# Kernel optimization log

Measured on AMD Instinct MI355X. Metric: run time of the kernel, lower is better.

Reference implementation:

```python
import jax, jax.numpy as jnp
import numpy as np

N = 10000      # num nodes
DEG = 8        # avg out-degree
E = N * DEG    # num bonds (directed edges)
D_IN = 128; D_HID = 128; D_OUT = 128; H = 16; HD = D_OUT // H
NG = 20; G_STOP = 10.0   # GaussianSmearing: 20 gaussians on [0, 10]
NF = 3                   # AngularEncoding num_funcs -> 1 + 4*NF = 13 feats


def _triplets(row, col, n):
    # numpy replica of BondUpdateLayer.triplets (SparseTensor version):
    # for each edge e=(j=row[e] -> i=col[e]), enumerate edges e'=(k -> j), drop k==i.
    order = np.argsort(col, kind='stable')          # edges sorted by target node
    in_count = np.bincount(col, minlength=n)
    in_start = np.concatenate([np.zeros(1, np.int64), np.cumsum(in_count)])
    num_t = in_count[row]                           # triplets per edge e
    T = int(num_t.sum())
    idx_ji = np.repeat(np.arange(row.size), num_t)
    within = np.arange(T) - np.repeat(np.cumsum(num_t) - num_t, num_t)
    idx_kj = order[in_start[row[idx_ji]] + within]
    idx_k = row[idx_kj]
    idx_i = col[idx_ji]
    idx_j = row[idx_ji]
    mask = idx_i != idx_k
    return idx_i[mask], idx_j[mask], idx_k[mask], idx_kj[mask], idx_ji[mask]


def setup_inputs() -> dict:
    key = jax.random.key(0)
    ks = jax.random.split(key, 8)
    rng = np.random.default_rng(0)
    src = np.repeat(np.arange(N), DEG)
    dst = (src + rng.integers(1, N, size=E)) % N    # random targets, never self-loop
    i_i, i_j, i_k, i_kj, i_ji = _triplets(src, dst, N)
    kv_dim = D_IN + 2 * NG + (1 + 4 * NF)           # 128 + 40 + 13 = 181

    def mlp_params(k, din):
        k1, k2 = jax.random.split(k)
        return {
            'W1': jax.random.normal(k1, (din, D_HID)) * 0.05, 'b1': jnp.zeros(D_HID),
            'g': jnp.ones(D_HID), 'b': jnp.zeros(D_HID),
            'W2': jax.random.normal(k2, (D_HID, D_OUT)) * 0.05, 'b2': jnp.zeros(D_OUT),
        }

    inp = {
        'h': jax.random.normal(ks[3], (N, D_IN)),
        'h_bond': jax.random.normal(ks[4], (E, D_IN)),
        'pos': jax.random.normal(ks[5], (N, 3)) * 3.0,
    }
    for name, k, din in (('hk', ks[0], kv_dim), ('hv', ks[1], kv_dim), ('hq', ks[2], D_IN)):
        for pn, v in mlp_params(k, din).items():
            inp[f'{name}_{pn}'] = v
    inp['bond_row'] = jnp.asarray(src, jnp.int32)
    inp['bond_col'] = jnp.asarray(dst, jnp.int32)
    inp['idx_i'] = jnp.asarray(i_i, jnp.int32)
    inp['idx_j'] = jnp.asarray(i_j, jnp.int32)
    inp['idx_k'] = jnp.asarray(i_k, jnp.int32)
    inp['idx_kj'] = jnp.asarray(i_kj, jnp.int32)
    inp['idx_ji'] = jnp.asarray(i_ji, jnp.int32)
    return inp


def _gauss(d):
    off = jnp.linspace(0.0, G_STOP, NG)
    coeff = -0.5 / (off[1] - off[0]) ** 2
    return jnp.exp(coeff * (d[:, None] - off) ** 2)


def _ang(a):
    freqs = jnp.asarray([1.0, 2.0, 3.0, 1.0, 0.5, 1.0 / 3.0])   # [i+1] + [1/(i+1)]
    x = a[:, None] * freqs
    return jnp.concatenate([a[:, None], jnp.sin(x), jnp.cos(x)], -1)


def _mlp(x, W1, b1, g, b, W2, b2):
    # Linear -> LayerNorm -> ReLU -> Linear
    hdn = x @ W1 + b1
    mu = hdn.mean(-1, keepdims=True)
    var = ((hdn - mu) ** 2).mean(-1, keepdims=True)
    hdn = jax.nn.relu(g * (hdn - mu) * jax.lax.rsqrt(var + 1e-5) + b)
    return hdn @ W2 + b2


def _forward(h, h_bond, pos,
             hk_W1, hk_b1, hk_g, hk_b, hk_W2, hk_b2,
             hv_W1, hv_b1, hv_g, hv_b, hv_W2, hv_b2,
             hq_W1, hq_b1, hq_g, hq_b, hq_W2, hq_b2,
             bond_row, bond_col, idx_i, idx_j, idx_k, idx_kj, idx_ji):
    # per-edge distance features (i=col, j=row in the torch code)
    dist = jnp.linalg.norm(pos[bond_col] - pos[bond_row], axis=-1)   # [E]
    r_feat = _gauss(dist)                                            # [E, 20]
    # per-triplet angle features
    pi = pos[idx_i]
    pji = pos[idx_j] - pi
    pki = pos[idx_k] - pi
    a = (pji * pki).sum(-1)
    bcr = jnp.linalg.norm(jnp.cross(pji, pki), axis=-1)
    a_feat = _ang(jnp.arctan2(bcr, a))                               # [T, 13]
    kv = jnp.concatenate([h_bond[idx_kj], r_feat[idx_kj], r_feat[idx_ji], a_feat], -1)  # [T, 181]
    T = kv.shape[0]
    k = _mlp(kv, hk_W1, hk_b1, hk_g, hk_b, hk_W2, hk_b2).reshape(T, H, HD)
    v = _mlp(kv, hv_W1, hv_b1, hv_g, hv_b, hv_W2, hv_b2).reshape(T, H, HD)
    q = _mlp(h_bond[idx_ji], hq_W1, hq_b1, hq_g, hq_b, hq_W2, hq_b2).reshape(T, H, HD)
    logits = (q * k).sum(-1) / np.sqrt(HD)                           # [T, H]
    # scatter_softmax over idx_ji (segments = edges)
    mx = jax.ops.segment_max(logits, idx_ji, num_segments=E)
    ex = jnp.exp(logits - mx[idx_ji])
    den = jax.ops.segment_sum(ex, idx_ji, num_segments=E)
    alpha = ex / den[idx_ji]                                         # [T, H]
    out = jax.ops.segment_sum(alpha[:, :, None] * v, idx_ji, num_segments=E)  # [E, H, HD]
    return out.reshape(E, D_OUT)


def reference(h, h_bond, pos,
              hk_W1, hk_b1, hk_g, hk_b, hk_W2, hk_b2,
              hv_W1, hv_b1, hv_g, hv_b, hv_W2, hv_b2,
              hq_W1, hq_b1, hq_g, hq_b, hq_W2, hq_b2,
              bond_row, bond_col, idx_i, idx_j, idx_k, idx_kj, idx_ji):
    return _forward(h, h_bond, pos,
                    hk_W1, hk_b1, hk_g, hk_b, hk_W2, hk_b2,
                    hv_W1, hv_b1, hv_g, hv_b, hv_W2, hv_b2,
                    hq_W1, hq_b1, hq_g, hq_b, hq_W2, hq_b2,
                    bond_row, bond_col, idx_i, idx_j, idx_k, idx_kj, idx_ji)
```

## Files before the change

kernel.cpp:

```cpp
#include <hip/hip_runtime.h>
#include <hip/hip_bf16.h>
#include <math.h>

typedef __hip_bfloat16 bf16;
typedef unsigned int u32;

__device__ __forceinline__ float b2f(bf16 x){ return __bfloat162float(x); }
__device__ __forceinline__ bf16  f2b(float x){ return __float2bfloat16(x); }
__device__ __forceinline__ float lo16(u32 u){ return __uint_as_float(u << 16); }
__device__ __forceinline__ float hi16(u32 u){ return __uint_as_float(u & 0xFFFF0000u); }
__device__ __forceinline__ u32 bfbits(float x){
    u32 u = __float_as_uint(x);
    return (u + 0x7FFFu + ((u >> 16) & 1u)) >> 16;
}

#define RSQRT8 0.35355339059327373f
#define G_STEP (10.0f/19.0f)
#define G_COEF (-0.5f/(G_STEP*G_STEP))

__device__ __forceinline__ constexpr int PERM4(int h){
    return ((h&1)<<3) | ((h&2)<<1) | ((h&4)>>1) | ((h&8)>>3);
}

__device__ __forceinline__ float fast_atan2(float y, float x){
    float ax = fabsf(x);
    float mn = fminf(y, ax), mx = fmaxf(y, ax);
    float t = mn / fmaxf(mx, 1e-30f);
    float s = t*t;
    float p = t * (0.99997726f + s*(-0.33262347f + s*(0.19354346f +
              s*(-0.11643287f + s*(0.05265332f + s*(-0.01172120f))))));
    float r = (y > ax) ? (1.5707963267948966f - p) : p;
    r = (x < 0.f) ? (3.14159265358979323f - r) : r;
    return r;
}


__global__ void seg_start_kernel(const int* __restrict__ idx_ji, int T,
                                 int* __restrict__ seg, int E)
{
    int e = blockIdx.x * blockDim.x + threadIdx.x;
    if (e > E) return;
    int lo = 0, hi = T;
    while (lo < hi) { int mid = (lo + hi) >> 1; if (idx_ji[mid] < e) lo = mid + 1; else hi = mid; }
    seg[e] = lo;
}

__global__ void marker_kernel(float* out, int n){
    int i = blockIdx.x * blockDim.x + threadIdx.x;
    if (i < n) out[i] = 12345.0f;
}

__global__ void pack_w2(const float* __restrict__ Wk2, const float* __restrict__ Wv2,
                        u32* __restrict__ kw2t, u32* __restrict__ vw2t)
{
    int idx = blockIdx.x*256 + threadIdx.x;
    if (idx >= 8192) return;
    int c = idx >> 6, p = idx & 63;
    kw2t[idx] = bfbits(Wk2[(size_t)(2*p)*128 + c]) | (bfbits(Wk2[(size_t)(2*p+1)*128 + c]) << 16);
    int j = idx >> 7, o = idx & 127;
    vw2t[idx] = bfbits(Wv2[(size_t)(2*j)*128 + o]) | (bfbits(Wv2[(size_t)(2*j+1)*128 + o]) << 16);
}

__global__ __launch_bounds__(128) void q_kernel(
    const float* __restrict__ W1, const float* __restrict__ B1,
    const float* __restrict__ G,  const float* __restrict__ Bln,
    const float* __restrict__ W2, const float* __restrict__ B2,
    const float* __restrict__ h_bond, bf16* __restrict__ qout, int E)
{
    __shared__ u32 sW[128*65];
    __shared__ float sH[16][130];
    __shared__ float sX[128];
    __shared__ float sRed[4];
    int tid = threadIdx.x; int wv = tid>>6, lane = tid&63;
    int base = blockIdx.x * 16;

    for (int idx = tid; idx < 128*128; idx += 128) {
        int i = idx >> 7, d = idx & 127;
        ((bf16*)sW)[d*130 + i] = f2b(W1[idx]);
    }
    __syncthreads();
    for (int ei = 0; ei < 16; ++ei) {
        int e = base + ei; if (e >= E) break;
        sX[tid] = h_bond[(size_t)e*128 + tid];
        __syncthreads();
        float acc = B1[tid];
        const u32* wrow = &sW[tid*65];
        #pragma unroll 8
        for (int j = 0; j < 64; ++j) {
            u32 w = wrow[j];
            acc += sX[2*j]*lo16(w) + sX[2*j+1]*hi16(w);
        }
        float s1 = acc, s2 = acc*acc;
        for (int m = 1; m < 64; m <<= 1) { s1 += __shfl_xor(s1, m, 64); s2 += __shfl_xor(s2, m, 64); }
        if (lane == 0) { sRed[wv*2] = s1; sRed[wv*2+1] = s2; }
        __syncthreads();
        float tot = sRed[0] + sRed[2], tot2 = sRed[1] + sRed[3];
        float mu = tot * (1.f/128.f);
        float var = fmaxf(tot2 * (1.f/128.f) - mu*mu, 0.f);
        float nv = G[tid] * (acc - mu) * rsqrtf(var + 1e-5f) + Bln[tid];
        sH[ei][tid] = fmaxf(nv, 0.f);
        __syncthreads();
    }
    __syncthreads();
    for (int idx = tid; idx < 128*128; idx += 128) {
        int i = idx >> 7, d = idx & 127;
        ((bf16*)sW)[d*130 + i] = f2b(W2[idx]);
    }
    __syncthreads();
    for (int ei = 0; ei < 16; ++ei) {
        int e = base + ei; if (e >= E) break;
        float acc = B2[tid];
        const u32* wrow = &sW[tid*65];
        #pragma unroll 8
        for (int j = 0; j < 64; ++j) {
            u32 w = wrow[j];
            acc += sH[ei][2*j]*lo16(w) + sH[ei][2*j+1]*hi16(w);
        }
        qout[(size_t)e*128 + tid] = f2b(acc);
    }
}

__global__ __launch_bounds__(128) void p_prep(
    const float* __restrict__ W1, const float* __restrict__ h_bond,
    const float* __restrict__ pos, const int* __restrict__ row,
    const int* __restrict__ col, bf16* __restrict__ P1, int E)
{
    __shared__ u32 sW[128*75];
    __shared__ float sX[4][152];
    int tid = threadIdx.x;
    for (int idx = tid; idx < 148*128; idx += 128) {
        int i = idx >> 7, d = idx & 127;
        ((bf16*)sW)[d*150 + i] = f2b(W1[idx]);
    }
    __syncthreads();
    int base = blockIdx.x * 16;
    for (int e4 = 0; e4 < 16; e4 += 4) {
        #pragma unroll
        for (int q = 0; q < 4; ++q) {
            int e = base + e4 + q;
            sX[q][tid] = (e < E) ? h_bond[(size_t)e*128 + tid] : 0.f;
        }
        if (tid < 80) {
            int q = tid / 20, g = tid % 20;
            int e = base + e4 + q;
            float rf = 0.f;
            if (e < E) {
                int i0 = col[e], j0 = row[e];
                float dx = pos[(size_t)i0*3+0] - pos[(size_t)j0*3+0];
                float dy = pos[(size_t)i0*3+1] - pos[(size_t)j0*3+1];
                float dz = pos[(size_t)i0*3+2] - pos[(size_t)j0*3+2];
                float dist = sqrtf(dx*dx + dy*dy + dz*dz);
                float t = dist - (float)g * G_STEP;
                rf = __expf(G_COEF * t * t);
            }
            sX[q][128 + g] = rf;
        }
        __syncthreads();
        float acc0 = 0.f, acc1 = 0.f, acc2 = 0.f, acc3 = 0.f;
        const u32* wrow = &sW[tid*75];
        #pragma unroll 4
        for (int j = 0; j < 74; ++j) {
            u32 w = wrow[j]; float wl = lo16(w), wh = hi16(w);
            acc0 += sX[0][2*j]*wl + sX[0][2*j+1]*wh;
            acc1 += sX[1][2*j]*wl + sX[1][2*j+1]*wh;
            acc2 += sX[2][2*j]*wl + sX[2][2*j+1]*wh;
            acc3 += sX[3][2*j]*wl + sX[3][2*j+1]*wh;
        }
        int e = base + e4;
        if (e   < E) P1[(size_t)e*128     + tid] = f2b(acc0);
        if (e+1 < E) P1[(size_t)(e+1)*128 + tid] = f2b(acc1);
        if (e+2 < E) P1[(size_t)(e+2)*128 + tid] = f2b(acc2);
        if (e+3 < E) P1[(size_t)(e+3)*128 + tid] = f2b(acc3);
        __syncthreads();
    }
}

#define EDGE_SETUP(W1full, b1v_, P2a_, P2b_, wa_) \
    float P2a_ = b1v_.x, P2b_ = b1v_.y; \
    { const float2* wbp = (const float2*)((W1full) + (size_t)148*128); \
      for (int g2 = 0; g2 < 20; ++g2) { \
        float tg = dist - (float)g2 * G_STEP; \
        float rf = __expf(G_COEF * tg * tg); \
        float2 wb = wbp[g2*64 + lane]; \
        P2a_ += rf * wb.x; \
        P2b_ += rf * wb.y; \
      } } \
    u32 wa_[13]; \
    { const float2* wap = (const float2*)((W1full) + (size_t)168*128); \
      _Pragma("unroll") \
      for (int f_ = 0; f_ < 13; ++f_) { \
        float2 w = wap[f_*64 + lane]; \
        wa_[f_] = bfbits(w.x) | (bfbits(w.y) << 16); \
      } }

__global__ __launch_bounds__(256, 3) void fused_kernel(
    const u32* __restrict__ kw2t, const u32* __restrict__ vw2t,
    const float* __restrict__ Wk1, const float* __restrict__ Bk1,
    const float* __restrict__ Gkg, const float* __restrict__ Bkln,
    const float* __restrict__ Wv1, const float* __restrict__ Bv1,
    const float* __restrict__ Gvg, const float* __restrict__ Bvln,
    const float* __restrict__ B2v,
    const bf16* __restrict__ qf, const bf16* __restrict__ P1k, const bf16* __restrict__ P1v,
    const float* __restrict__ pos, const int* __restrict__ seg,
    const int* __restrict__ idx_kj, const int* __restrict__ idx_k,
    const int* __restrict__ row, const int* __restrict__ col,
    float* __restrict__ out, int E)
{
    __shared__ u32 sS[4][16*66];
    int tid = threadIdx.x, lane = tid & 63, wv = tid >> 6;
    int e = __builtin_amdgcn_readfirstlane(blockIdx.x*4 + wv);
    if (e >= E) return;
    int s0 = __builtin_amdgcn_readfirstlane(seg[e]);
    int s1 = __builtin_amdgcn_readfirstlane(seg[e+1]);
    if (s1 <= s0) { out[(size_t)e*128 + lane] = 0.f; out[(size_t)e*128 + 64 + lane] = 0.f; return; }

    float2 b1k = ((const float2*)Bk1)[lane];
    float2 gk  = ((const float2*)Gkg)[lane];
    float2 bk  = ((const float2*)Bkln)[lane];
    float2 b1v = ((const float2*)Bv1)[lane];
    float2 gv  = ((const float2*)Gvg)[lane];
    float2 bv  = ((const float2*)Bvln)[lane];

    int i0 = __builtin_amdgcn_readfirstlane(col[e]);
    int j0 = __builtin_amdgcn_readfirstlane(row[e]);
    float pix = pos[(size_t)i0*3+0], piy = pos[(size_t)i0*3+1], piz = pos[(size_t)i0*3+2];
    float pjx = pos[(size_t)j0*3+0], pjy = pos[(size_t)j0*3+1], pjz = pos[(size_t)j0*3+2];
    float dxx = pix-pjx, dyy = piy-pjy, dzz = piz-pjz;
    float dist = sqrtf(dxx*dxx + dyy*dyy + dzz*dzz);

    EDGE_SETUP(Wk1, b1k, P2ak, P2bk, wak);
    EDGE_SETUP(Wv1, b1v, P2av, P2bv, wav);

    float Gk0[16], Gk1[16];
    const u32* qrow = (const u32*)(qf + (size_t)e*128);
    #pragma unroll
    for (int h = 0; h < 16; ++h) {
        float g0 = 0.f, g1 = 0.f;
        #pragma unroll
        for (int j = 0; j < 4; ++j) {
            u32 qp = qrow[h*4 + j];
            float ql = lo16(qp), qh = hi16(qp);
            u32 w0 = kw2t[(h*8 + 2*j)*64 + lane];
            u32 w1 = kw2t[(h*8 + 2*j + 1)*64 + lane];
            g0 += ql*lo16(w0) + qh*lo16(w1);
            g1 += ql*hi16(w0) + qh*hi16(w1);
        }
        Gk0[h] = g0; Gk1[h] = g1;
    }

    float S0[16], S1[16];
    #pragma unroll
    for (int h = 0; h < 16; ++h) { S0[h] = 0.f; S1[h] = 0.f; }
    float m = -1e30f, sden = 0.f;

    const u32* p1ku = (const u32*)P1k;
    const u32* p1vu = (const u32*)P1v;
    float ax = pjx-pix, ay = pjy-piy, az = pjz-piz;

    int kj_p = __builtin_amdgcn_readfirstlane(idx_kj[s0]);
    int kn_p = __builtin_amdgcn_readfirstlane(idx_k[s0]);
    u32 ppk_p = p1ku[(size_t)kj_p*64 + lane];
    u32 ppv_p = p1vu[(size_t)kj_p*64 + lane];
    float pkx = pos[(size_t)kn_p*3+0], pky = pos[(size_t)kn_p*3+1], pkz = pos[(size_t)kn_p*3+2];

    for (int t = s0; t < s1; ++t) {
        u32 ppk = ppk_p, ppv = ppv_p;
        float bx = pkx-pix, by = pky-piy, bz = pkz-piz;
        int tn = (t+1 < s1) ? (t+1) : t;
        kj_p = __builtin_amdgcn_readfirstlane(idx_kj[tn]);
        kn_p = __builtin_amdgcn_readfirstlane(idx_k[tn]);
        ppk_p = p1ku[(size_t)kj_p*64 + lane];
        ppv_p = p1vu[(size_t)kj_p*64 + lane];
        pkx = pos[(size_t)kn_p*3+0]; pky = pos[(size_t)kn_p*3+1]; pkz = pos[(size_t)kn_p*3+2];

        float dt = ax*bx + ay*by + az*bz;
        float cx = ay*bz - az*by, cy = az*bx - ax*bz, cz = ax*by - ay*bx;
        float bcr = sqrtf(cx*cx + cy*cy + cz*cz);
        float ang = fast_atan2(bcr, dt);
        float s1a = __sinf(ang),          c1a = __cosf(ang);
        float sh  = __sinf(0.5f*ang),     ch  = __cosf(0.5f*ang);
        float st3 = __sinf((1.f/3.f)*ang), ct3 = __cosf((1.f/3.f)*ang);
        float s2a = 2.f*s1a*c1a, c2a = 1.f - 2.f*s1a*s1a;
        float s3a = s1a*(3.f - 4.f*s1a*s1a), c3a = c1a*(4.f*c1a*c1a - 3.f);
        float af[13] = {ang, s1a, s2a, s3a, s1a, sh, st3, c1a, c2a, c3a, c1a, ch, ct3};

        float v0A = P2ak + lo16(ppk), v1A = P2bk + hi16(ppk);
        float v0B = P2av + lo16(ppv), v1B = P2bv + hi16(ppv);
        #pragma unroll
        for (int f = 0; f < 13; ++f) {
            u32 wkp = wak[f], wvp = wav[f];
            v0A += af[f]*lo16(wkp); v1A += af[f]*hi16(wkp);
            v0B += af[f]*lo16(wvp); v1B += af[f]*hi16(wvp);
        }
        float sumA = v0A + v1A, ssqA = v0A*v0A + v1A*v1A;
        float sumB = v0B + v1B, ssqB = v0B*v0B + v1B*v1B;
        float rA = ((lane&1) ? ssqA : sumA) + __shfl_xor((lane&1) ? sumA : ssqA, 1, 64);
        float rB = ((lane&1) ? ssqB : sumB) + __shfl_xor((lane&1) ? sumB : ssqB, 1, 64);
        rA += __shfl_xor(rA, 2, 64);  rB += __shfl_xor(rB, 2, 64);
        rA += __shfl_xor(rA, 4, 64);  rB += __shfl_xor(rB, 4, 64);
        rA += __shfl_xor(rA, 8, 64);  rB += __shfl_xor(rB, 8, 64);
        rA += __shfl_xor(rA, 16, 64); rB += __shfl_xor(rB, 16, 64);
        rA += __shfl_xor(rA, 32, 64); rB += __shfl_xor(rB, 32, 64);
        float oA = __shfl_xor(rA, 1, 64), oB = __shfl_xor(rB, 1, 64);
        float totA  = (lane&1) ? oA : rA, tot2A = (lane&1) ? rA : oA;
        float totB  = (lane&1) ? oB : rB, tot2B = (lane&1) ? rB : oB;
        float muA = totA * (1.f/128.f);
        float muB = totB * (1.f/128.f);
        float varA = fmaxf(tot2A * (1.f/128.f) - muA*muA, 0.f);
        float varB = fmaxf(tot2B * (1.f/128.f) - muB*muB, 0.f);
        float rsA = rsqrtf(varA + 1e-5f), rsB = rsqrtf(varB + 1e-5f);
        float h0A = fmaxf(gk.x*(v0A-muA)*rsA + bk.x, 0.f);
        float h1A = fmaxf(gk.y*(v1A-muA)*rsA + bk.y, 0.f);
        float h0B = fmaxf(gv.x*(v0B-muB)*rsB + bv.x, 0.f);
        float h1B = fmaxf(gv.y*(v1B-muB)*rsB + bv.y, 0.f);

        float p[16];
        #pragma unroll
        for (int h = 0; h < 16; ++h) p[h] = h0A*Gk0[h] + h1A*Gk1[h];
        float a8[8];
        { int up = lane & 1;
          #pragma unroll
          for (int i = 0; i < 8; ++i) {
            float kp = up ? p[i+8] : p[i];
            float sd = up ? p[i]   : p[i+8];
            a8[i] = kp + __shfl_xor(sd, 1, 64);
          } }
        float a4[4];
        { int up = lane & 2;
          #pragma unroll
          for (int i = 0; i < 4; ++i) {
            float kp = up ? a8[i+4] : a8[i];
            float sd = up ? a8[i]   : a8[i+4];
            a4[i] = kp + __shfl_xor(sd, 2, 64);
          } }
        float a2[2];
        { int up = lane & 4;
          #pragma unroll
          for (int i = 0; i < 2; ++i) {
            float kp = up ? a4[i+2] : a4[i];
            float sd = up ? a4[i]   : a4[i+2];
            a2[i] = kp + __shfl_xor(sd, 4, 64);
          } }
        float a1;
        { int up = lane & 8;
          float kp = up ? a2[1] : a2[0];
          float sd = up ? a2[0] : a2[1];
          a1 = kp + __shfl_xor(sd, 8, 64);
        }
        a1 += __shfl_xor(a1, 16, 64);
        a1 += __shfl_xor(a1, 32, 64);
        float lg = a1 * RSQRT8;

        if (__any(lg > m + 8.f)) {
            float nm = fmaxf(m, lg);
            float fac = __expf(m - nm);
            sden *= fac; m = nm;
            #pragma unroll
            for (int h = 0; h < 16; ++h) {
                float fh = __shfl(fac, PERM4(h), 64);
                S0[h] *= fh; S1[h] *= fh;
            }
        }
        float ex = __expf(lg - m);
        sden += ex;
        #pragma unroll
        for (int h = 0; h < 16; ++h) {
            float alh = __shfl(ex, PERM4(h), 64);
            S0[h] += alh*h0B; S1[h] += alh*h1B;
        }
    }

    float inv = 1.f / sden;
    #pragma unroll
    for (int h = 0; h < 16; ++h) {
        float sc = __shfl(inv, PERM4(h), 64);
        sS[wv][h*66 + lane] = bfbits(S0[h]*sc) | (bfbits(S1[h]*sc) << 16);
    }
    __threadfence_block();
    int h0i = lane >> 3, h1i = 8 + (lane >> 3);
    float acc0 = B2v[lane], acc1 = B2v[lane + 64];
    const u32* sr0 = &sS[wv][h0i*66];
    const u32* sr1 = &sS[wv][h1i*66];
    #pragma unroll 8
    for (int j = 0; j < 64; ++j) {
        u32 us0 = sr0[j], uw0 = vw2t[j*128 + lane];
        u32 us1 = sr1[j], uw1 = vw2t[j*128 + 64 + lane];
        acc0 += lo16(us0)*lo16(uw0) + hi16(us0)*hi16(uw0);
        acc1 += lo16(us1)*lo16(uw1) + hi16(us1)*hi16(uw1);
    }
    out[(size_t)e*128 + lane] = acc0;
    out[(size_t)e*128 + 64 + lane] = acc1;
}

extern "C" void kernel_launch(void* const* d_in, const int* in_sizes, int n_in,
                              void* d_out, int out_size, void* d_ws, size_t ws_size,
                              hipStream_t stream)
{
    const float* h_bond = (const float*)d_in[1];
    const float* pos    = (const float*)d_in[2];
    const float* hkW1 = (const float*)d_in[3];
    const float* hkb1 = (const float*)d_in[4];
    const float* hkg  = (const float*)d_in[5];
    const float* hkb  = (const float*)d_in[6];
    const float* hkW2 = (const float*)d_in[7];
    const float* hvW1 = (const float*)d_in[9];
    const float* hvb1 = (const float*)d_in[10];
    const float* hvg  = (const float*)d_in[11];
    const float* hvb  = (const float*)d_in[12];
    const float* hvW2 = (const float*)d_in[13];
    const float* hvb2 = (const float*)d_in[14];
    const float* hqW1 = (const float*)d_in[15];
    const float* hqb1 = (const float*)d_in[16];
    const float* hqg  = (const float*)d_in[17];
    const float* hqb  = (const float*)d_in[18];
    const float* hqW2 = (const float*)d_in[19];
    const float* hqb2 = (const float*)d_in[20];
    const int* row    = (const int*)d_in[21];
    const int* col    = (const int*)d_in[22];
    const int* idx_k  = (const int*)d_in[25];
    const int* idx_kj = (const int*)d_in[26];
    const int* idx_ji = (const int*)d_in[27];

    int E = in_sizes[21];
    int T = in_sizes[27];

    char* w = (char*)d_ws;
    size_t off = 0;
    auto carve = [&](size_t bytes) -> void* {
        void* p = w + off;
        off = (off + bytes + 255) & ~(size_t)255;
        return p;
    };
    int*  seg   = (int*) carve(((size_t)E + 1) * sizeof(int));
    bf16* qf    = (bf16*)carve((size_t)E * 128 * sizeof(bf16));
    bf16* P1k   = (bf16*)carve((size_t)E * 128 * sizeof(bf16));
    bf16* P1v   = (bf16*)carve((size_t)E * 128 * sizeof(bf16));
    u32*  kw2t  = (u32*) carve(8192 * sizeof(u32));
    u32*  vw2t  = (u32*) carve(8192 * sizeof(u32));

    if (off > ws_size) {
        marker_kernel<<<(out_size + 255)/256, 256, 0, stream>>>((float*)d_out, out_size);
        return;
    }

    int gq = (E + 15)/16;
    int gw = (E + 3)/4;
    seg_start_kernel<<<(E + 1 + 255)/256, 256, 0, stream>>>(idx_ji, T, seg, E);
    pack_w2<<<32, 256, 0, stream>>>(hkW2, hvW2, kw2t, vw2t);
    q_kernel<<<gq, 128, 0, stream>>>(hqW1, hqb1, hqg, hqb, hqW2, hqb2, h_bond, qf, E);
    p_prep<<<gq, 128, 0, stream>>>(hkW1, h_bond, pos, row, col, P1k, E);
    p_prep<<<gq, 128, 0, stream>>>(hvW1, h_bond, pos, row, col, P1v, E);
    fused_kernel<<<gw, 256, 0, stream>>>(kw2t, vw2t,
        hkW1, hkb1, hkg, hkb,
        hvW1, hvb1, hvg, hvb,
        hvb2, qf, P1k, P1v, pos, seg, idx_kj, idx_k, row, col, (float*)d_out, E);
}
```

Measured before the change: 1.795 ms.

## Batch q_kernel over four edges, fold duplicate angular weights, pack Gk to bf16

New measurement: 3.063 ms. 1.71x slower.

```diff
diff --git a/kernel.cpp b/kernel.cpp
--- a/kernel.cpp
+++ b/kernel.cpp
@@ -69,8 +69,8 @@
 {
     __shared__ u32 sW[128*65];
     __shared__ float sH[16][130];
-    __shared__ float sX[128];
-    __shared__ float sRed[4];
+    __shared__ float sX[4][130];
+    __shared__ float sRed[4][4];
     int tid = threadIdx.x; int wv = tid>>6, lane = tid&63;
     int base = blockIdx.x * 16;
 
@@ -79,44 +79,71 @@
         ((bf16*)sW)[d*130 + i] = f2b(W1[idx]);
     }
     __syncthreads();
-    for (int ei = 0; ei < 16; ++ei) {
-        int e = base + ei; if (e >= E) break;
-        sX[tid] = h_bond[(size_t)e*128 + tid];
+    for (int e4 = 0; e4 < 16; e4 += 4) {
+        #pragma unroll
+        for (int q = 0; q < 4; ++q) {
+            int e = base + e4 + q;
+            sX[q][tid] = (e < E) ? h_bond[(size_t)e*128 + tid] : 0.f;
+        }
         __syncthreads();
-        float acc = B1[tid];
+        float b1t = B1[tid];
+        float ac[4] = {b1t, b1t, b1t, b1t};
         const u32* wrow = &sW[tid*65];
-        #pragma unroll 8
+        #pragma unroll 4
         for (int j = 0; j < 64; ++j) {
-            u32 w = wrow[j];
-            acc += sX[2*j]*lo16(w) + sX[2*j+1]*hi16(w);
-        }
-        float s1 = acc, s2 = acc*acc;
-        for (int m = 1; m < 64; m <<= 1) { s1 += __shfl_xor(s1, m, 64); s2 += __shfl_xor(s2, m, 64); }
-        if (lane == 0) { sRed[wv*2] = s1; sRed[wv*2+1] = s2; }
+            u32 w = wrow[j]; float wl = lo16(w), wh = hi16(w);
+            #pragma unroll
+            for (int q = 0; q < 4; ++q)
+                ac[q] += sX[q][2*j]*wl + sX[q][2*j+1]*wh;
+        }
+        float s1v[4], s2v[4];
+        #pragma unroll
+        for (int q = 0; q < 4; ++q) { s1v[q] = ac[q]; s2v[q] = ac[q]*ac[q]; }
+        #pragma unroll
+        for (int m = 1; m < 64; m <<= 1) {
+            #pragma unroll
+            for (int q = 0; q < 4; ++q) {
+                s1v[q] += __shfl_xor(s1v[q], m, 64);
+                s2v[q] += __shfl_xor(s2v[q], m, 64);
+            }
+        }
+        if (lane == 0) {
+            #pragma unroll
+            for (int q = 0; q < 4; ++q) { sRed[q][wv*2] = s1v[q]; sRed[q][wv*2+1] = s2v[q]; }
+        }
         __syncthreads();
-        float tot = sRed[0] + sRed[2], tot2 = sRed[1] + sRed[3];
-        float mu = tot * (1.f/128.f);
-        float var = fmaxf(tot2 * (1.f/128.f) - mu*mu, 0.f);
-        float nv = G[tid] * (acc - mu) * rsqrtf(var + 1e-5f) + Bln[tid];
-        sH[ei][tid] = fmaxf(nv, 0.f);
+        float gt = G[tid], bt = Bln[tid];
+        #pragma unroll
+        for (int q = 0; q < 4; ++q) {
+            float tot = sRed[q][0] + sRed[q][2], tot2 = sRed[q][1] + sRed[q][3];
+            float mu = tot * (1.f/128.f);
+            float var = fmaxf(tot2 * (1.f/128.f) - mu*mu, 0.f);
+            float nv = gt * (ac[q] - mu) * rsqrtf(var + 1e-5f) + bt;
+            sH[e4+q][tid] = fmaxf(nv, 0.f);
+        }
         __syncthreads();
     }
-    __syncthreads();
     for (int idx = tid; idx < 128*128; idx += 128) {
         int i = idx >> 7, d = idx & 127;
         ((bf16*)sW)[d*130 + i] = f2b(W2[idx]);
     }
     __syncthreads();
-    for (int ei = 0; ei < 16; ++ei) {
-        int e = base + ei; if (e >= E) break;
-        float acc = B2[tid];
+    for (int e4 = 0; e4 < 16; e4 += 4) {
+        float b2t = B2[tid];
+        float ac[4] = {b2t, b2t, b2t, b2t};
         const u32* wrow = &sW[tid*65];
-        #pragma unroll 8
+        #pragma unroll 4
         for (int j = 0; j < 64; ++j) {
-            u32 w = wrow[j];
-            acc += sH[ei][2*j]*lo16(w) + sH[ei][2*j+1]*hi16(w);
-        }
-        qout[(size_t)e*128 + tid] = f2b(acc);
+            u32 w = wrow[j]; float wl = lo16(w), wh = hi16(w);
+            #pragma unroll
+            for (int q = 0; q < 4; ++q)
+                ac[q] += sH[e4+q][2*j]*wl + sH[e4+q][2*j+1]*wh;
+        }
+        #pragma unroll
+        for (int q = 0; q < 4; ++q) {
+            int e = base + e4 + q;
+            if (e < E) qout[(size_t)e*128 + tid] = f2b(ac[q]);
+        }
     }
 }
 
@@ -185,15 +212,34 @@
         P2a_ += rf * wb.x; \
         P2b_ += rf * wb.y; \
       } } \
-    u32 wa_[13]; \
+    u32 wa_[11]; \
     { const float2* wap = (const float2*)((W1full) + (size_t)168*128); \
-      _Pragma("unroll") \
-      for (int f_ = 0; f_ < 13; ++f_) { \
-        float2 w = wap[f_*64 + lane]; \
-        wa_[f_] = bfbits(w.x) | (bfbits(w.y) << 16); \
-      } }
-
-__global__ __launch_bounds__(256, 3) void fused_kernel(
+      float2 w0  = wap[ 0*64 + lane]; \
+      float2 w1  = wap[ 1*64 + lane]; \
+      float2 w2  = wap[ 2*64 + lane]; \
+      float2 w3  = wap[ 3*64 + lane]; \
+      float2 w4  = wap[ 4*64 + lane]; \
+      float2 w5  = wap[ 5*64 + lane]; \
+      float2 w6  = wap[ 6*64 + lane]; \
+      float2 w7  = wap[ 7*64 + lane]; \
+      float2 w8  = wap[ 8*64 + lane]; \
+      float2 w9  = wap[ 9*64 + lane]; \
+      float2 w10 = wap[10*64 + lane]; \
+      float2 w11 = wap[11*64 + lane]; \
+      float2 w12 = wap[12*64 + lane]; \
+      wa_[0]  = bfbits(w0.x)        | (bfbits(w0.y)        << 16); \
+      wa_[1]  = bfbits(w1.x+w4.x)   | (bfbits(w1.y+w4.y)   << 16); \
+      wa_[2]  = bfbits(w2.x)        | (bfbits(w2.y)        << 16); \
+      wa_[3]  = bfbits(w3.x)        | (bfbits(w3.y)        << 16); \
+      wa_[4]  = bfbits(w5.x)        | (bfbits(w5.y)        << 16); \
+      wa_[5]  = bfbits(w6.x)        | (bfbits(w6.y)        << 16); \
+      wa_[6]  = bfbits(w7.x+w10.x)  | (bfbits(w7.y+w10.y)  << 16); \
+      wa_[7]  = bfbits(w8.x)        | (bfbits(w8.y)        << 16); \
+      wa_[8]  = bfbits(w9.x)        | (bfbits(w9.y)        << 16); \
+      wa_[9]  = bfbits(w11.x)       | (bfbits(w11.y)       << 16); \
+      wa_[10] = bfbits(w12.x)       | (bfbits(w12.y)       << 16); }
+
+__global__ __launch_bounds__(256, 4) void fused_kernel(
     const u32* __restrict__ kw2t, const u32* __restrict__ vw2t,
     const float* __restrict__ Wk1, const float* __restrict__ Bk1,
     const float* __restrict__ Gkg, const float* __restrict__ Bkln,
@@ -231,21 +277,23 @@
     EDGE_SETUP(Wk1, b1k, P2ak, P2bk, wak);
     EDGE_SETUP(Wv1, b1v, P2av, P2bv, wav);
 
-    float Gk0[16], Gk1[16];
-    const u32* qrow = (const u32*)(qf + (size_t)e*128);
-    #pragma unroll
-    for (int h = 0; h < 16; ++h) {
-        float g0 = 0.f, g1 = 0.f;
-        #pragma unroll
-        for (int j = 0; j < 4; ++j) {
-            u32 qp = qrow[h*4 + j];
-            float ql = lo16(qp), qh = hi16(qp);
-            u32 w0 = kw2t[(h*8 + 2*j)*64 + lane];
-            u32 w1 = kw2t[(h*8 + 2*j + 1)*64 + lane];
-            g0 += ql*lo16(w0) + qh*lo16(w1);
-            g1 += ql*hi16(w0) + qh*hi16(w1);
-        }
-        Gk0[h] = g0; Gk1[h] = g1;
+    u32 Gkp[16];
+    {
+        const u32* qrow = (const u32*)(qf + (size_t)e*128);
+        #pragma unroll
+        for (int h = 0; h < 16; ++h) {
+            float g0 = 0.f, g1 = 0.f;
+            #pragma unroll
+            for (int j = 0; j < 4; ++j) {
+                u32 qp = qrow[h*4 + j];
+                float ql = lo16(qp), qh = hi16(qp);
+                u32 w0 = kw2t[(h*8 + 2*j)*64 + lane];
+                u32 w1 = kw2t[(h*8 + 2*j + 1)*64 + lane];
+                g0 += ql*lo16(w0) + qh*lo16(w1);
+                g1 += ql*hi16(w0) + qh*hi16(w1);
+            }
+            Gkp[h] = bfbits(g0) | (bfbits(g1) << 16);
+        }
     }
 
     float S0[16], S1[16];
@@ -275,19 +323,23 @@
 
         float dt = ax*bx + ay*by + az*bz;
         float cx = ay*bz - az*by, cy = az*bx - ax*bz, cz = ax*by - ay*bx;
-        float bcr = sqrtf(cx*cx + cy*cy + cz*cz);
+        float bcr2 = cx*cx + cy*cy + cz*cz;
+        float bcr = sqrtf(bcr2);
+        float inv_h = rsqrtf(fmaxf(dt*dt + bcr2, 1e-30f));
+        float c1a = dt * inv_h;
+        float s1a = bcr * inv_h;
         float ang = fast_atan2(bcr, dt);
-        float s1a = __sinf(ang),          c1a = __cosf(ang);
-        float sh  = __sinf(0.5f*ang),     ch  = __cosf(0.5f*ang);
-        float st3 = __sinf((1.f/3.f)*ang), ct3 = __cosf((1.f/3.f)*ang);
+        float sh  = sqrtf(fmaxf(0.5f*(1.f - c1a), 0.f));
+        float ch  = sqrtf(fmaxf(0.5f*(1.f + c1a), 0.f));
+        float st3, ct3; __sincosf((1.f/3.f)*ang, &st3, &ct3);
         float s2a = 2.f*s1a*c1a, c2a = 1.f - 2.f*s1a*s1a;
         float s3a = s1a*(3.f - 4.f*s1a*s1a), c3a = c1a*(4.f*c1a*c1a - 3.f);
-        float af[13] = {ang, s1a, s2a, s3a, s1a, sh, st3, c1a, c2a, c3a, c1a, ch, ct3};
+        float af[11] = {ang, s1a, s2a, s3a, sh, st3, c1a, c2a, c3a, ch, ct3};
 
         float v0A = P2ak + lo16(ppk), v1A = P2bk + hi16(ppk);
         float v0B = P2av + lo16(ppv), v1B = P2bv + hi16(ppv);
         #pragma unroll
-        for (int f = 0; f < 13; ++f) {
+        for (int f = 0; f < 11; ++f) {
             u32 wkp = wak[f], wvp = wav[f];
             v0A += af[f]*lo16(wkp); v1A += af[f]*hi16(wkp);
             v0B += af[f]*lo16(wvp); v1B += af[f]*hi16(wvp);
@@ -316,7 +368,10 @@
 
         float p[16];
         #pragma unroll
-        for (int h = 0; h < 16; ++h) p[h] = h0A*Gk0[h] + h1A*Gk1[h];
+        for (int h = 0; h < 16; ++h) {
+            u32 g = Gkp[h];
+            p[h] = h0A*lo16(g) + h1A*hi16(g);
+        }
         float a8[8];
         { int up = lane & 1;
           #pragma unroll
```
